# Optimization experiments

Measured on AMD Instinct MI355X. Metric: run time of the kernel, lower is better.

Reference implementation:

```python
import jax, jax.numpy as jnp
import numpy as np

B, C_IN, N, K, UP = 4, 128, 1024, 9, 4
EPS_BN = 1e-5


def _grid():
    # gen_grid(4): num_x=num_y=2, linspace(-0.2,0.2,2) -> (4,2)
    g = jnp.linspace(-0.2, 0.2, 2)
    x, y = jnp.meshgrid(g, g, indexing='ij')
    return jnp.stack([x, y], axis=-1).reshape(-1, 2)


def _knn(x, k, dilation):
    # x: (B,C,N). L2-normalize features, matrix pairwise dist, top-k, dilated select.
    nrm = jnp.sqrt(jnp.sum(x * x, axis=1, keepdims=True))
    xn = x / jnp.maximum(nrm, 1e-12)
    xt = xn.transpose(0, 2, 1)                      # (B,N,C)
    sq = jnp.sum(xt * xt, axis=-1)                  # (B,N)
    dist = sq[:, :, None] - 2.0 * jnp.einsum('bnc,bmc->bnm', xt, xt) + sq[:, None, :]
    _, idx = jax.lax.top_k(-dist, k * dilation)     # k*d nearest (incl. self)
    return idx[:, :, ::dilation]                    # (B,N,k)


def _bn(x, g, b, axes):
    # training-mode batchnorm over given axes, channel axis = 1
    m = jnp.mean(x, axis=axes, keepdims=True)
    v = jnp.mean((x - m) ** 2, axis=axes, keepdims=True)
    sh = [1] * x.ndim
    sh[1] = -1
    return (x - m) * jax.lax.rsqrt(v + EPS_BN) * g.reshape(sh) + b.reshape(sh)


def _edge_conv(x, k, dil, W, g, b):
    # DGCNN edge conv: gather neighbors, [x_i, x_j-x_i], 1x1 conv, BN, relu, max over k
    idx = _knn(x, k, dil)                                        # (B,N,k)
    x_j = jax.vmap(lambda xx, ii: xx[:, ii])(x, idx)             # (B,C,N,k)
    x_i = jnp.broadcast_to(x[..., None], x_j.shape)
    feat = jnp.concatenate([x_i, x_j - x_i], axis=1)             # (B,2C,N,k)
    out = jnp.einsum('oc,bcnk->bonk', W, feat)
    out = jax.nn.relu(_bn(out, g, b, (0, 2, 3)))
    return jnp.max(out, axis=-1)                                 # (B,Cout,N)


def _conv1d(x, W, b):
    return jnp.einsum('oc,bcn->bon', W, x) + b[None, :, None]


def _atten(x, Wf, bf, gf, bef, Wg, bg, gg, beg, Wh, bh, gh, beh, gamma):
    # attention_unit / RA_Layer1 math (C=130)
    f = jax.nn.relu(_bn(_conv1d(x, Wf, bf), gf, bef, (0, 2)))    # (B,C/4,M)
    g_ = jax.nn.relu(_bn(_conv1d(x, Wg, bg), gg, beg, (0, 2)))
    h = jax.nn.relu(_bn(_conv1d(x, Wh, bh), gh, beh, (0, 2)))    # (B,C,M)
    s = jnp.einsum('bcn,bcm->bnm', g_, f)                        # g^T @ f: (B,M,M)
    beta = jax.nn.softmax(s, axis=2)
    o = jnp.einsum('bcn,bnm->bcm', h, beta)                      # h @ beta
    return gamma * o + x


def _forward(inp, Wa, gna, bta, Wb, gnb, btb, Wf, bf, gf, bef, Wg, bg, gg, beg,
             Wh, bh, gh, beh, gamma, W1, b1, W2, b2):
    x1 = _edge_conv(inp, K, 1, Wa, gna, bta)                     # (B,256,N)
    x2 = _edge_conv(inp, K, 2, Wb, gnb, btb)                     # (B,256,N)
    x = jnp.concatenate([x1, x2], axis=1)                        # (B,512,N)
    net = x.transpose(0, 2, 1).reshape(B, N * UP, 128)           # (B,4N,128)
    grid = jnp.repeat(_grid(), N, axis=0)                        # (4N,2)
    grid = jnp.broadcast_to(grid[None], (B, N * UP, 2)).astype(net.dtype)
    net = jnp.concatenate([net, grid], axis=2).transpose(0, 2, 1)  # (B,130,4N)
    net = _atten(net, Wf, bf, gf, bef, Wg, bg, gg, beg, Wh, bh, gh, beh, gamma)
    net = jax.nn.relu(_conv1d(net, W1, b1))                      # 130->256
    net = jax.nn.relu(_conv1d(net, W2, b2))                      # 256->128
    return net                                                   # (B,128,4N)


def setup_inputs() -> dict:
    key = jax.random.key(0)
    ks = jax.random.split(key, 24)
    rn = lambda k, sh, s=0.05: jax.random.normal(k, sh, jnp.float32) * s
    d = {
        'inp': jax.random.normal(ks[0], (B, C_IN, N), jnp.float32),
        'Wa': rn(ks[1], (256, 256)), 'gna': 1.0 + rn(ks[2], (256,)), 'bta': rn(ks[3], (256,)),
        'Wb': rn(ks[4], (256, 256)), 'gnb': 1.0 + rn(ks[5], (256,)), 'btb': rn(ks[6], (256,)),
        'Wf': rn(ks[7], (32, 130)), 'bf': rn(ks[8], (32,)), 'gf': 1.0 + rn(ks[9], (32,)), 'bef': rn(ks[9], (32,)),
        'Wg': rn(ks[10], (32, 130)), 'bg': rn(ks[11], (32,)), 'gg': 1.0 + rn(ks[12], (32,)), 'beg': rn(ks[12], (32,)),
        'Wh': rn(ks[13], (130, 130)), 'bh': rn(ks[14], (130,)), 'gh': 1.0 + rn(ks[15], (130,)), 'beh': rn(ks[15], (130,)),
        'gamma': rn(ks[16], (), 1.0),
        'W1': rn(ks[17], (256, 130)), 'b1': rn(ks[18], (256,)),
        'W2': rn(ks[19], (128, 256)), 'b2': rn(ks[20], (128,)),
    }
    return d


def reference(inp, Wa, gna, bta, Wb, gnb, btb, Wf, bf, gf, bef, Wg, bg, gg, beg,
              Wh, bh, gh, beh, gamma, W1, b1, W2, b2):
    return _forward(inp, Wa, gna, bta, Wb, gnb, btb, Wf, bf, gf, bef, Wg, bg, gg, beg,
                    Wh, bh, gh, beh, gamma, W1, b1, W2, b2)
```

## Files before the change

kernel.cpp:

```cpp
#include <hip/hip_runtime.h>

namespace {
constexpr int NB = 4;
constexpr int CI = 128;
constexpr int NP = 1024;
constexpr int MM = 4096;
constexpr float EPSBN = 1e-5f;
constexpr float LOG2E = 1.4426950408889634f;

constexpr size_t OPS_SH = 2162688;
constexpr size_t OFF_OP   = 0;
constexpr size_t OFF_DIST = 0;
constexpr size_t OFF_PM   = 0;
constexpr size_t OFF_QM   = 2097152;
constexpr size_t OFF_HRAW = 0;
constexpr size_t OFF_FGRAW= 2359296;
constexpr size_t OFF_Y1   = 0;
constexpr size_t OFF_FGT  = 6488064;
constexpr size_t OFF_HB   = 7012352;
constexpr size_t OFF_A16  = 6488064;
constexpr size_t OFF_X16  = 8192000;
constexpr size_t OFF_LSE  = 9502720;
constexpr size_t OFF_LSEP = 9519104;
constexpr size_t OFF_STATS= 9650176;
constexpr size_t OFF_ABE  = 9715712;
constexpr size_t OFF_ABFG = 9716736;
constexpr size_t OFF_ABH  = 9716864;
constexpr size_t OFF_FGP  = 9717376;
constexpr size_t OFF_BIAS = 9725568;
constexpr size_t OFF_W16  = 9726208;
constexpr size_t OFF_KNN  = 9779712;
constexpr size_t OFF_XN   = 9853440;
constexpr size_t OFF_SQ   = 10377728;
constexpr size_t W16_FG = 0;
constexpr size_t W16_H  = 10240;
constexpr size_t W16_C1 = 33280;
constexpr size_t W16_C2 = 74240;
constexpr size_t B_FG = 0, B_H = 64, B_C1 = 208, B_C2 = 464;
}

typedef __attribute__((ext_vector_type(8))) short short8;
typedef __attribute__((ext_vector_type(4))) float f32x4;
#define MFMA16(A, B, C) __builtin_amdgcn_mfma_f32_16x16x32_bf16(A, B, C, 0, 0, 0)

__device__ inline unsigned short f2bf(float x) {
  unsigned int u = __float_as_uint(x);
  unsigned int r = u + 0x7fff + ((u >> 16) & 1);
  return (unsigned short)(r >> 16);
}
__device__ inline float bf2f(unsigned short s) {
  return __uint_as_float(((unsigned int)s) << 16);
}

__global__ __launch_bounds__(256) void k_prep(const float* __restrict__ Wf, const float* __restrict__ Wg,
                                              const float* __restrict__ Wh, const float* __restrict__ W1,
                                              const float* __restrict__ W2, const float* __restrict__ bf,
                                              const float* __restrict__ bg, const float* __restrict__ bh,
                                              const float* __restrict__ b1, const float* __restrict__ b2,
                                              unsigned short* __restrict__ W16, float* __restrict__ BIAS) {
  int i = blockIdx.x * 256 + threadIdx.x;
  if (i < 107008) {
    float v = 0.f;
    if (i < 10240) { int o = i / 160, c = i % 160; if (c < 130) v = (o < 32) ? Wf[o * 130 + c] : Wg[(o - 32) * 130 + c]; }
    else if (i < 33280) { int r = i - 10240; int o = r / 160, c = r % 160; if (o < 130 && c < 130) v = Wh[o * 130 + c]; }
    else if (i < 74240) { int r = i - 33280; int o = r / 160, c = r % 160; if (c < 130) v = W1[o * 130 + c]; }
    else { int r = i - 74240; int o = r / 256, c = r % 256; v = W2[o * 256 + c]; }
    W16[i] = f2bf(v);
  } else if (i < 107648) {
    int j = i - 107008; float v = 0.f;
    if (j < 64) v = (j < 32) ? bf[j] : bg[j - 32];
    else if (j < 208) { int c = j - 64; if (c < 130) v = bh[c]; }
    else if (j < 464) v = b1[j - 208];
    else if (j < 592) v = b2[j - 464];
    BIAS[j] = v;
  }
}

__global__ __launch_bounds__(256) void k_norm(const float* __restrict__ x,
                                              float* __restrict__ xn,
                                              float* __restrict__ sq) {
  int t = blockIdx.x * 256 + threadIdx.x;
  int b = t >> 10, n = t & 1023;
  const float* xb = x + (size_t)b * CI * NP + n;
  float ss = 0.f;
  #pragma unroll 4
  for (int c = 0; c < CI; ++c) { float v = xb[(size_t)c * NP]; ss += v * v; }
  float inv = 1.f / fmaxf(sqrtf(ss), 1e-12f);
  float* xo = xn + (size_t)b * CI * NP + n;
  float s2 = 0.f;
  #pragma unroll 4
  for (int c = 0; c < CI; ++c) { float v = xb[(size_t)c * NP] * inv; xo[(size_t)c * NP] = v; s2 += v * v; }
  sq[t] = s2;
}

__global__ __launch_bounds__(256) void k_dist(const float* __restrict__ xn,
                                              const float* __restrict__ sq,
                                              float* __restrict__ dist) {
  __shared__ float As[32][68], Bs[32][68];
  int t = threadIdx.x;
  int m0 = blockIdx.x * 64, n0 = blockIdx.y * 64, b = blockIdx.z;
  int mg = t & 15, ng = t >> 4;
  float acc[16];
  #pragma unroll
  for (int i = 0; i < 16; ++i) acc[i] = 0.f;
  for (int cc = 0; cc < 128; cc += 32) {
    __syncthreads();
    for (int idx = t; idx < 2048; idx += 256) {
      int c = idx >> 6, j = idx & 63;
      As[c][j] = xn[((size_t)b * CI + cc + c) * NP + n0 + j];
      Bs[c][j] = xn[((size_t)b * CI + cc + c) * NP + m0 + j];
    }
    __syncthreads();
    #pragma unroll
    for (int c = 0; c < 32; ++c) {
      float4 avv = *(const float4*)&As[c][ng * 4];
      float4 bvv = *(const float4*)&Bs[c][mg * 4];
      float a[4] = {avv.x, avv.y, avv.z, avv.w};
      float bb[4] = {bvv.x, bvv.y, bvv.z, bvv.w};
      #pragma unroll
      for (int i = 0; i < 4; ++i)
        #pragma unroll
        for (int j = 0; j < 4; ++j) acc[i * 4 + j] += a[i] * bb[j];
    }
  }
  #pragma unroll
  for (int i = 0; i < 4; ++i) {
    int n = n0 + ng * 4 + i;
    float sn = sq[b * NP + n];
    float4 r;
    r.x = sn + sq[b * NP + m0 + mg * 4 + 0] - 2.f * acc[i * 4 + 0];
    r.y = sn + sq[b * NP + m0 + mg * 4 + 1] - 2.f * acc[i * 4 + 1];
    r.z = sn + sq[b * NP + m0 + mg * 4 + 2] - 2.f * acc[i * 4 + 2];
    r.w = sn + sq[b * NP + m0 + mg * 4 + 3] - 2.f * acc[i * 4 + 3];
    *(float4*)&dist[((size_t)b * NP + n) * NP + m0 + mg * 4] = r;
  }
}

__global__ __launch_bounds__(64) void k_knn(const float* __restrict__ dist,
                                            int* __restrict__ knn) {
  int row = blockIdx.x;
  int l = threadIdx.x;
  const float* dr = dist + (size_t)row * NP;
  float d[16];
  #pragma unroll
  for (int i = 0; i < 16; ++i) d[i] = dr[l + 64 * i];
  for (int s = 0; s < 18; ++s) {
    float best = __builtin_inff(); int bslot = -1;
    #pragma unroll
    for (int i = 0; i < 16; ++i) if (d[i] < best) { best = d[i]; bslot = i; }
    int bidx = (bslot >= 0) ? (l + 64 * bslot) : 0x7fffffff;
    float bd = best; int bi = bidx;
    #pragma unroll
    for (int off = 32; off > 0; off >>= 1) {
      float od = __shfl_xor(bd, off);
      int   oi = __shfl_xor(bi, off);
      if (od < bd || (od == bd && oi < bi)) { bd = od; bi = oi; }
    }
    if (l == 0) knn[row * 18 + s] = bi;
    if ((bi & 63) == l) d[bi >> 6] = __builtin_inff();
  }
}

__global__ __launch_bounds__(256) void k_pq(const float* __restrict__ x,
                                            const float* __restrict__ Wa,
                                            const float* __restrict__ Wb,
                                            float* __restrict__ Pm,
                                            float* __restrict__ Qm) {
  __shared__ float Xs[32][68], Wp[32][68], Wq[32][68];
  int t = threadIdx.x;
  int nt = blockIdx.x, ot = blockIdx.y, bz = blockIdx.z;
  int b = bz >> 1, e = bz & 1;
  const float* W = e ? Wb : Wa;
  int eb = e * 4 + b;
  int mg = t & 15, og = t >> 4;
  float accp[16], accq[16];
  #pragma unroll
  for (int i = 0; i < 16; ++i) { accp[i] = 0.f; accq[i] = 0.f; }
  for (int cc = 0; cc < 128; cc += 32) {
    __syncthreads();
    for (int idx = t; idx < 2048; idx += 256) {
      int c = idx >> 6, n = idx & 63;
      Xs[c][n] = x[((size_t)b * CI + cc + c) * NP + nt * 64 + n];
    }
    for (int idx = t; idx < 2048; idx += 256) {
      int o = idx >> 5, c = idx & 31;
      float w1 = W[(ot * 64 + o) * 256 + cc + c];
      float w2 = W[(ot * 64 + o) * 256 + 128 + cc + c];
      Wp[c][o] = w1 - w2; Wq[c][o] = w2;
    }
    __syncthreads();
    #pragma unroll
    for (int c = 0; c < 32; ++c) {
      float4 xv = *(const float4*)&Xs[c][mg * 4];
      float4 wp = *(const float4*)&Wp[c][og * 4];
      float4 wq = *(const float4*)&Wq[c][og * 4];
      float xa[4] = {xv.x, xv.y, xv.z, xv.w};
      float pa[4] = {wp.x, wp.y, wp.z, wp.w};
      float qa[4] = {wq.x, wq.y, wq.z, wq.w};
      #pragma unroll
      for (int i = 0; i < 4; ++i)
        #pragma unroll
        for (int j = 0; j < 4; ++j) { accp[i * 4 + j] += pa[i] * xa[j]; accq[i * 4 + j] += qa[i] * xa[j]; }
    }
  }
  #pragma unroll
  for (int j = 0; j < 4; ++j) {
    int n = nt * 64 + mg * 4 + j;
    int o0 = ot * 64 + og * 4;
    float4 rp = {accp[j], accp[4 + j], accp[8 + j], accp[12 + j]};
    float4 rq = {accq[j], accq[4 + j], accq[8 + j], accq[12 + j]};
    *(float4*)&Pm[((size_t)eb * 1024 + n) * 256 + o0] = rp;
    *(float4*)&Qm[((size_t)eb * 1024 + n) * 256 + o0] = rq;
  }
}

__global__ __launch_bounds__(256) void k_edge_stats(const float* __restrict__ Pm,
                                                    const float* __restrict__ Qm,
                                                    const int* __restrict__ knn,
                                                    float* __restrict__ stats) {
  int o = threadIdx.x;
  int chunk = blockIdx.x, b = blockIdx.y, e = blockIdx.z;
  int eb = e * 4 + b;
  float s = 0.f, s2 = 0.f;
  for (int nn = 0; nn < 64; ++nn) {
    int n = chunk * 64 + nn;
    float p = Pm[((size_t)eb * 1024 + n) * 256 + o];
    const int* kn = knn + (b * 1024 + n) * 18;
    #pragma unroll
    for (int kk = 0; kk < 9; ++kk) {
      int j = kn[e ? 2 * kk : kk];
      float v = p + Qm[((size_t)eb * 1024 + j) * 256 + o];
      s += v; s2 += v * v;
    }
  }
  size_t idx = ((((size_t)e * 4 + b) * 16 + chunk) * 256 + o) * 2;
  stats[idx] = s; stats[idx + 1] = s2;
}

__global__ __launch_bounds__(256) void k_edge_fin(const float* __restrict__ stats,
                                                  const float* __restrict__ gna, const float* __restrict__ bta,
                                                  const float* __restrict__ gnb, const float* __restrict__ btb,
                                                  float* __restrict__ ab) {
  int i = blockIdx.x * 256 + threadIdx.x;
  if (i >= 512) return;
  int e = i >> 8, o = i & 255;
  float s = 0.f, s2 = 0.f;
  for (int b = 0; b < 4; ++b)
    for (int ch = 0; ch < 16; ++ch) {
      size_t idx = ((((size_t)e * 4 + b) * 16 + ch) * 256 + o) * 2;
      s += stats[idx]; s2 += stats[idx + 1];
    }
  float cnt = 4.0f * 1024.0f * 9.0f;
  float mean = s / cnt;
  float var = s2 / cnt - mean * mean;
  float g = e ? gnb[o] : gna[o];
  float bt = e ? btb[o] : bta[o];
  float alpha = g * rsqrtf(var + EPSBN);
  ab[i * 2] = alpha; ab[i * 2 + 1] = bt - mean * alpha;
}

__global__ __launch_bounds__(256) void k_edge_apply(const float* __restrict__ Pm,
                                                    const float* __restrict__ Qm,
                                                    const int* __restrict__ knn,
                                                    const float* __restrict__ ab,
                                                    unsigned short* __restrict__ X16) {
  __shared__ int knl[18];
  int t = threadIdx.x;
  int n = blockIdx.x, b = blockIdx.y;
  if (t < 18) knl[t] = knn[(b * 1024 + n) * 18 + t];
  __syncthreads();
  int e = t >> 7, oo = t & 127;
  int eb = e * 4 + b;
  const float* Pr = Pm + ((size_t)eb * 1024 + n) * 256;
  const float* Qb = Qm + (size_t)eb * 1024 * 256;
  float p0 = Pr[oo], p1 = Pr[oo + 128];
  float a0 = ab[(e * 256 + oo) * 2], be0 = ab[(e * 256 + oo) * 2 + 1];
  float a1 = ab[(e * 256 + oo + 128) * 2], be1 = ab[(e * 256 + oo + 128) * 2 + 1];
  float mx0 = -__builtin_inff(), mx1 = -__builtin_inff();
  #pragma unroll
  for (int kk = 0; kk < 9; ++kk) {
    int j = knl[e ? 2 * kk : kk];
    const float* Qr = Qb + (size_t)j * 256;
    mx0 = fmaxf(mx0, fmaf(a0, p0 + Qr[oo], be0));
    mx1 = fmaxf(mx1, fmaf(a1, p1 + Qr[oo + 128], be1));
  }
  int u0 = e << 1, u1 = (e << 1) | 1;
  X16[((size_t)b * MM + 4 * n + u0) * 160 + oo] = f2bf(fmaxf(mx0, 0.f));
  X16[((size_t)b * MM + 4 * n + u1) * 160 + oo] = f2bf(fmaxf(mx1, 0.f));
  if (t < 128) {
    int u = t >> 5, c = 128 + (t & 31);
    int gr = n >> 8;
    float v = (c == 128) ? ((gr < 2) ? -0.2f : 0.2f) : (c == 129) ? ((gr & 1) ? 0.2f : -0.2f) : 0.f;
    X16[((size_t)b * MM + 4 * n + u) * 160 + c] = f2bf(v);
  }
}

template <int KSTEPS, int CTPER, int OUTMODE, bool RELU>
__global__ __launch_bounds__(256) void k_convm(const unsigned short* __restrict__ src,
                                               const unsigned short* __restrict__ W16,
                                               const float* __restrict__ bias,
                                               float* __restrict__ dstF,
                                               unsigned short* __restrict__ dstB,
                                               int outld, int rows) {
  constexpr int LD = KSTEPS * 32;
  int t = threadIdx.x; int w = t >> 6; int l = t & 63;
  int lm = l & 15, g = l >> 4;
  int b = blockIdx.z; int ct0 = blockIdx.y * CTPER;
  int srow = blockIdx.x * 64 + w * 16 + lm;
  const unsigned short* sp = src + ((size_t)b * MM + srow) * LD + 8 * g;
  const unsigned short* wp = W16 + ((size_t)ct0 * 16 + lm) * LD + 8 * g;
  f32x4 acc[CTPER];
  #pragma unroll
  for (int i = 0; i < CTPER; ++i) acc[i] = {0.f, 0.f, 0.f, 0.f};
  #pragma unroll
  for (int cc = 0; cc < KSTEPS; ++cc) {
    short8 bfr = *(const short8*)(sp + cc * 32);
    #pragma unroll
    for (int ct = 0; ct < CTPER; ++ct) {
      short8 af = *(const short8*)(wp + (size_t)ct * 16 * LD + cc * 32);
      acc[ct] = MFMA16(af, bfr, acc[ct]);
    }
  }
  #pragma unroll
  for (int ct = 0; ct < CTPER; ++ct) {
    int o0 = (ct0 + ct) * 16 + 4 * g;
    float4 bv = *(const float4*)&bias[o0];
    float v[4] = {acc[ct][0] + bv.x, acc[ct][1] + bv.y, acc[ct][2] + bv.z, acc[ct][3] + bv.w};
    if (RELU) { v[0] = fmaxf(v[0], 0.f); v[1] = fmaxf(v[1], 0.f); v[2] = fmaxf(v[2], 0.f); v[3] = fmaxf(v[3], 0.f); }
    if (OUTMODE == 0) {
      float4 r = {v[0], v[1], v[2], v[3]};
      *(float4*)&dstF[((size_t)b * MM + srow) * outld + o0] = r;
    } else if (OUTMODE == 1) {
      uint2 pk;
      pk.x = (unsigned)f2bf(v[0]) | ((unsigned)f2bf(v[1]) << 16);
      pk.y = (unsigned)f2bf(v[2]) | ((unsigned)f2bf(v[3]) << 16);
      *(uint2*)&dstB[((size_t)b * MM + srow) * outld + o0] = pk;
    } else {
      #pragma unroll
      for (int r = 0; r < 4; ++r)
        dstF[((size_t)b * rows + o0 + r) * MM + srow] = v[r];
    }
  }
}

__global__ __launch_bounds__(256) void k_fgstats(const float* __restrict__ FGraw,
                                                 float* __restrict__ FGP) {
  __shared__ float red[4][64][2];
  int t = threadIdx.x; int c = t & 63, rq = t >> 6;
  int blk = blockIdx.x;
  float s = 0.f, s2 = 0.f;
  for (int k = 0; k < 64; ++k) {
    int r = blk * 256 + rq + 4 * k;
    float v = FGraw[(size_t)r * 64 + c];
    s += v; s2 += v * v;
  }
  red[rq][c][0] = s; red[rq][c][1] = s2;
  __syncthreads();
  if (t < 64) {
    float a = 0.f, a2 = 0.f;
    #pragma unroll
    for (int q = 0; q < 4; ++q) { a += red[q][t][0]; a2 += red[q][t][1]; }
    FGP[((size_t)blk * 64 + t) * 2] = a; FGP[((size_t)blk * 64 + t) * 2 + 1] = a2;
  }
}

__global__ __launch_bounds__(64) void k_fgfin(const float* __restrict__ FGP,
                                              const float* __restrict__ gf, const float* __restrict__ bef,
                                              const float* __restrict__ gg, const float* __restrict__ beg,
                                              float* __restrict__ ab) {
  int c = threadIdx.x;
  float s = 0.f, s2 = 0.f;
  for (int blk = 0; blk < 64; ++blk) { s += FGP[((size_t)blk * 64 + c) * 2]; s2 += FGP[((size_t)blk * 64 + c) * 2 + 1]; }
  float cnt = 16384.f;
  float mean = s / cnt, var = s2 / cnt - mean * mean;
  float gv = (c < 32) ? gf[c] : gg[c - 32];
  float bv = (c < 32) ? bef[c] : beg[c - 32];
  float alpha = gv * rsqrtf(var + EPSBN);
  ab[c * 2] = alpha; ab[c * 2 + 1] = bv - mean * alpha;
}

__global__ __launch_bounds__(256) void k_bnstats(const float* __restrict__ src,
                                                 const float* __restrict__ g,
                                                 const float* __restrict__ be,
                                                 float* __restrict__ ab, int ldC) {
  int o = blockIdx.x;
  int t = threadIdx.x;
  float s = 0.f, s2 = 0.f;
  for (int b = 0; b < NB; ++b) {
    const float* r = src + ((size_t)b * ldC + o) * MM;
    for (int m = t; m < MM; m += 256) { float v = r[m]; s += v; s2 += v * v; }
  }
  __shared__ float rs[256], rs2[256];
  rs[t] = s; rs2[t] = s2;
  __syncthreads();
  for (int off = 128; off > 0; off >>= 1) {
    if (t < off) { rs[t] += rs[t + off]; rs2[t] += rs2[t + off]; }
    __syncthreads();
  }
  if (t == 0) {
    float cnt = 16384.0f;
    float mean = rs[0] / cnt, var = rs2[0] / cnt - mean * mean;
    float alpha = g[o] * rsqrtf(var + EPSBN);
    ab[o * 2] = alpha; ab[o * 2 + 1] = be[o] - mean * alpha;
  }
}

__global__ __launch_bounds__(256) void k_cvtFG(const float* __restrict__ FGraw,
                                               const float* __restrict__ ab,
                                               unsigned short* __restrict__ FGT) {
  int i = blockIdx.x * 256 + threadIdx.x;
  int row = i >> 3, c0 = (i & 7) * 8;
  float vv[8];
  float4 u0 = *(const float4*)&FGraw[(size_t)row * 64 + c0];
  float4 u1 = *(const float4*)&FGraw[(size_t)row * 64 + c0 + 4];
  vv[0] = u0.x; vv[1] = u0.y; vv[2] = u0.z; vv[3] = u0.w;
  vv[4] = u1.x; vv[5] = u1.y; vv[6] = u1.z; vv[7] = u1.w;
  uint4 pk;
  unsigned pw[4];
  #pragma unroll
  for (int h = 0; h < 4; ++h) {
    int c = c0 + 2 * h;
    float a0 = ab[c * 2], b0 = ab[c * 2 + 1];
    float a1 = ab[(c + 1) * 2], b1 = ab[(c + 1) * 2 + 1];
    float x0 = fmaxf(fmaf(a0, vv[2 * h], b0), 0.f);
    float x1 = fmaxf(fmaf(a1, vv[2 * h + 1], b1), 0.f);
    pw[h] = (unsigned)f2bf(x0) | ((unsigned)f2bf(x1) << 16);
  }
  pk.x = pw[0]; pk.y = pw[1]; pk.z = pw[2]; pk.w = pw[3];
  *(uint4*)&FGT[(size_t)row * 64 + c0] = pk;
}

__global__ __launch_bounds__(256) void k_cvtH(const float* __restrict__ src,
                                              const float* __restrict__ ab,
                                              unsigned short* __restrict__ dst) {
  int i = blockIdx.x * 256 + threadIdx.x;
  int m4 = i & 1023; int c = (i >> 10) % 144; int b = i / (144 * 1024);
  ushort4 ov = {0, 0, 0, 0};
  if (c < 130) {
    float4 v = *(const float4*)&src[((size_t)b * 144 + c) * MM + m4 * 4];
    float a = ab[c * 2], be = ab[c * 2 + 1];
    ov.x = f2bf(fmaxf(fmaf(a, v.x, be), 0.f));
    ov.y = f2bf(fmaxf(fmaf(a, v.y, be), 0.f));
    ov.z = f2bf(fmaxf(fmaf(a, v.z, be), 0.f));
    ov.w = f2bf(fmaxf(fmaf(a, v.w, be), 0.f));
  }
  *(ushort4*)&dst[((size_t)b * 144 + c) * MM + m4 * 4] = ov;
}

__global__ __launch_bounds__(256) void k_zlse(const unsigned short* __restrict__ FGT,
                                              float* __restrict__ LSEP) {
  int t = threadIdx.x; int w = t >> 6; int l = t & 63;
  int b = blockIdx.z; int ms = blockIdx.y;
  int n0 = blockIdx.x * 64 + w * 16;
  int lm = l & 15, g = l >> 4;
  f32x4 z4 = {0.f, 0.f, 0.f, 0.f};
  short8 af = *(const short8*)&FGT[((size_t)b * MM + n0 + lm) * 64 + 32 + 8 * g];
  float rm[4], zz[4];
  #pragma unroll
  for (int r = 0; r < 4; ++r) { rm[r] = -__builtin_inff(); zz[r] = 0.f; }
  for (int it = 0; it < 16; ++it) {
    int m0 = ms * 1024 + it * 64;
    short8 bfr[4];
    #pragma unroll
    for (int mi = 0; mi < 4; ++mi)
      bfr[mi] = *(const short8*)&FGT[((size_t)b * MM + m0 + mi * 16 + lm) * 64 + 8 * g];
    #pragma unroll
    for (int mi = 0; mi < 4; ++mi) {
      f32x4 d = MFMA16(af, bfr[mi], z4);
      #pragma unroll
      for (int r = 0; r < 4; ++r) {
        float v = d[r] * LOG2E;
        float nm = fmaxf(rm[r], v);
        zz[r] = zz[r] * exp2f(rm[r] - nm) + exp2f(v - nm);
        rm[r] = nm;
      }
    }
  }
  #pragma unroll
  for (int off = 1; off < 16; off <<= 1) {
    #pragma unroll
    for (int r = 0; r < 4; ++r) {
      float om = __shfl_xor(rm[r], off);
      float oz = __shfl_xor(zz[r], off);
      float nm = fmaxf(rm[r], om);
      zz[r] = zz[r] * exp2f(rm[r] - nm) + oz * exp2f(om - nm);
      rm[r] = nm;
    }
  }
  if (lm == 0) {
    #pragma unroll
    for (int r = 0; r < 4; ++r) {
      int n = n0 + 4 * g + r;
      size_t idx = ((size_t)ms * 16384 + (size_t)b * MM + n) * 2;
      LSEP[idx] = rm[r]; LSEP[idx + 1] = zz[r];
    }
  }
}

__global__ __launch_bounds__(256) void k_lsered(const float* __restrict__ LSEP,
                                                float* __restrict__ LSE) {
  int bn = blockIdx.x * 256 + threadIdx.x;
  float rm = -__builtin_inff(), zz = 0.f;
  #pragma unroll
  for (int ms = 0; ms < 4; ++ms) {
    float m = LSEP[((size_t)ms * 16384 + bn) * 2];
    float z = LSEP[((size_t)ms * 16384 + bn) * 2 + 1];
    float nm = fmaxf(rm, m);
    zz = zz * exp2f(rm - nm) + z * exp2f(m - nm);
    rm = nm;
  }
  LSE[bn] = rm + log2f(zz);
}

__global__ __launch_bounds__(256) void k_omfma(const unsigned short* __restrict__ FGT,
                                               const unsigned short* __restrict__ HB,
                                               const float* __restrict__ LSE,
                                               unsigned short* __restrict__ Opart) {
  int t = threadIdx.x; int w = t >> 6; int l = t & 63;
  int b = blockIdx.y; int split = blockIdx.z;
  int lm = l & 15, g = l >> 4;
  int mcol0 = blockIdx.x * 128 + w * 32 + lm;
  int mcol1 = mcol0 + 16;
  f32x4 z4 = {0.f, 0.f, 0.f, 0.f};
  short8 Ff0 = *(const short8*)&FGT[((size_t)b * MM + mcol0) * 64 + 8 * g];
  short8 Ff1 = *(const short8*)&FGT[((size_t)b * MM + mcol1) * 64 + 8 * g];
  f32x4 acc0[9], acc1[9];
  #pragma unroll
  for (int ct = 0; ct < 9; ++ct) { acc0[ct] = z4; acc1[ct] = z4; }
  const int nchunks = (split < 2) ? 22 : 21;
  const int startc = split * 21 + ((split < 2) ? split : 2);
  const int start = startc * 32;
  const int end = start + nchunks * 32;
  const unsigned short* gptr = FGT + ((size_t)b * MM + lm) * 64 + 32 + 8 * g;
  const unsigned short* hbase = HB + ((size_t)b * 144 + lm) * MM + 8 * g;
  const float* lbase = LSE + (size_t)b * MM + 4 * g;
  int src01 = lm + 16 * (2 * (g & 1));
  int src23 = src01 + 16;
  bool hi = g >= 2;

  short8 a0 = *(const short8*)(gptr + (size_t)start * 64);
  short8 a1 = *(const short8*)(gptr + (size_t)(start + 16) * 64);
  float4 l0 = *(const float4*)(lbase + start);
  float4 l1 = *(const float4*)(lbase + start + 16);

  for (int n0 = start; n0 < end; n0 += 32) {
    const unsigned short* hp = hbase + n0;
    short8 hf[9];
    #pragma unroll
    for (int ct = 0; ct < 9; ++ct) hf[ct] = *(const short8*)(hp + (size_t)ct * 16 * MM);
    f32x4 s00 = MFMA16(a0, Ff0, z4);
    f32x4 s10 = MFMA16(a1, Ff0, z4);
    f32x4 s01 = MFMA16(a0, Ff1, z4);
    f32x4 s11 = MFMA16(a1, Ff1, z4);
    int nn = (n0 + 32 < end) ? (n0 + 32) : start;
    short8 na0 = *(const short8*)(gptr + (size_t)nn * 64);
    short8 na1 = *(const short8*)(gptr + (size_t)(nn + 16) * 64);
    float4 nl0 = *(const float4*)(lbase + nn);
    float4 nl1 = *(const float4*)(lbase + nn + 16);
    float le0[4] = {l0.x, l0.y, l0.z, l0.w};
    float le1[4] = {l1.x, l1.y, l1.z, l1.w};
    unsigned pk00[2], pk10[2], pk01[2], pk11[2];
    #pragma unroll
    for (int h2 = 0; h2 < 2; ++h2) {
      float e00a = exp2f(fmaf(s00[2 * h2], LOG2E, -le0[2 * h2]));
      float e00b = exp2f(fmaf(s00[2 * h2 + 1], LOG2E, -le0[2 * h2 + 1]));
      float e10a = exp2f(fmaf(s10[2 * h2], LOG2E, -le1[2 * h2]));
      float e10b = exp2f(fmaf(s10[2 * h2 + 1], LOG2E, -le1[2 * h2 + 1]));
      float e01a = exp2f(fmaf(s01[2 * h2], LOG2E, -le0[2 * h2]));
      float e01b = exp2f(fmaf(s01[2 * h2 + 1], LOG2E, -le0[2 * h2 + 1]));
      float e11a = exp2f(fmaf(s11[2 * h2], LOG2E, -le1[2 * h2]));
      float e11b = exp2f(fmaf(s11[2 * h2 + 1], LOG2E, -le1[2 * h2 + 1]));
      pk00[h2] = (unsigned)f2bf(e00a) | ((unsigned)f2bf(e00b) << 16);
      pk10[h2] = (unsigned)f2bf(e10a) | ((unsigned)f2bf(e10b) << 16);
      pk01[h2] = (unsigned)f2bf(e01a) | ((unsigned)f2bf(e01b) << 16);
      pk11[h2] = (unsigned)f2bf(e11a) | ((unsigned)f2bf(e11b) << 16);
    }
    a0 = na0; a1 = na1; l0 = nl0; l1 = nl1;
    unsigned a0w = (unsigned)__shfl((int)pk00[0], src01);
    unsigned b0w = (unsigned)__shfl((int)pk10[0], src01);
    unsigned a1w = (unsigned)__shfl((int)pk00[1], src01);
    unsigned b1w = (unsigned)__shfl((int)pk10[1], src01);
    unsigned a2w = (unsigned)__shfl((int)pk00[0], src23);
    unsigned b2w = (unsigned)__shfl((int)pk10[0], src23);
    unsigned a3w = (unsigned)__shfl((int)pk00[1], src23);
    unsigned b3w = (unsigned)__shfl((int)pk10[1], src23);
    union { unsigned u[4]; short8 s; } bu0;
    bu0.u[0] = hi ? b0w : a0w; bu0.u[1] = hi ? b1w : a1w;
    bu0.u[2] = hi ? b2w : a2w; bu0.u[3] = hi ? b3w : a3w;
    short8 bfrag0 = bu0.s;
    unsigned c0w = (unsigned)__shfl((int)pk01[0], src01);
    unsigned d0w = (unsigned)__shfl((int)pk11[0], src01);
    unsigned c1w = (unsigned)__shfl((int)pk01[1], src01);
    unsigned d1w = (unsigned)__shfl((int)pk11[1], src01);
    unsigned c2w = (unsigned)__shfl((int)pk01[0], src23);
    unsigned d2w = (unsigned)__shfl((int)pk11[0], src23);
    unsigned c3w = (unsigned)__shfl((int)pk01[1], src23);
    unsigned d3w = (unsigned)__shfl((int)pk11[1], src23);
    union { unsigned u[4]; short8 s; } bu1;
    bu1.u[0] = hi ? d0w : c0w; bu1.u[1] = hi ? d1w : c1w;
    bu1.u[2] = hi ? d2w : c2w; bu1.u[3] = hi ? d3w : c3w;
    short8 bfrag1 = bu1.s;
    #pragma unroll
    for (int ct = 0; ct < 9; ++ct) {
      acc0[ct] = MFMA16(hf[ct], bfrag0, acc0[ct]);
      acc1[ct] = MFMA16(hf[ct], bfrag1, acc1[ct]);
    }
  }
  unsigned short* op0 = Opart + (size_t)split * OPS_SH + ((size_t)b * MM + mcol0) * 132;
  unsigned short* op1 = Opart + (size_t)split * OPS_SH + ((size_t)b * MM + mcol1) * 132;
  #pragma unroll
  for (int ct = 0; ct < 9; ++ct) {
    int c0 = ct * 16 + 4 * g;
    if (c0 < 132) {
      uint2 p0, p1;
      p0.x = (unsigned)f2bf(acc0[ct][0]) | ((unsigned)f2bf(acc0[ct][1]) << 16);
      p0.y = (unsigned)f2bf(acc0[ct][2]) | ((unsigned)f2bf(acc0[ct][3]) << 16);
      p1.x = (unsigned)f2bf(acc1[ct][0]) | ((unsigned)f2bf(acc1[ct][1]) << 16);
      p1.y = (unsigned)f2bf(acc1[ct][2]) | ((unsigned)f2bf(acc1[ct][3]) << 16);
      *(uint2*)&op0[c0] = p0;
      *(uint2*)&op1[c0] = p1;
    }
  }
}

__global__ __launch_bounds__(256) void k_ored(const unsigned short* __restrict__ Op,
                                              const unsigned short* __restrict__ X16,
                                              const float* __restrict__ gma,
                                              unsigned short* __restrict__ A16) {
  int i = blockIdx.x * 256 + threadIdx.x;
  int row = i / 20, c8 = i % 20;
  int c0 = c8 * 8;
  unsigned short* ap = A16 + (size_t)row * 160 + c0;
  if (c0 >= 136) {
    uint4 z = {0, 0, 0, 0};
    *(uint4*)ap = z;
    return;
  }
  float gm = gma[0];
  float ov[8] = {0.f, 0.f, 0.f, 0.f, 0.f, 0.f, 0.f, 0.f};
  #pragma unroll
  for (int s = 0; s < 6; ++s) {
    const unsigned short* base = Op + (size_t)s * OPS_SH + (size_t)row * 132 + c0;
    uint2 u = *(const uint2*)base;
    ov[0] += bf2f((unsigned short)(u.x & 0xffff));
    ov[1] += bf2f((unsigned short)(u.x >> 16));
    ov[2] += bf2f((unsigned short)(u.y & 0xffff));
    ov[3] += bf2f((unsigned short)(u.y >> 16));
    if (c0 + 4 < 132) {
      uint2 v = *(const uint2*)(base + 4);
      ov[4] += bf2f((unsigned short)(v.x & 0xffff));
      ov[5] += bf2f((unsigned short)(v.x >> 16));
      ov[6] += bf2f((unsigned short)(v.y & 0xffff));
      ov[7] += bf2f((unsigned short)(v.y >> 16));
    }
  }
  short8 xv = *(const short8*)(X16 + (size_t)row * 160 + c0);
  unsigned pw[4];
  #pragma unroll
  for (int h = 0; h < 4; ++h) {
    int ca = c0 + 2 * h, cb = c0 + 2 * h + 1;
    float xa = bf2f((unsigned short)xv[2 * h]);
    float xb = bf2f((unsigned short)xv[2 * h + 1]);
    float va = (ca < 132) ? (gm * ov[2 * h] + xa) : 0.f;
    float vb = (cb < 132) ? (gm * ov[2 * h + 1] + xb) : 0.f;
    pw[h] = (unsigned)f2bf(va) | ((unsigned)f2bf(vb) << 16);
  }
  uint4 pk = {pw[0], pw[1], pw[2], pw[3]};
  *(uint4*)ap = pk;
}

extern "C" void kernel_launch(void* const* d_in, const int* in_sizes, int n_in,
                              void* d_out, int out_size, void* d_ws, size_t ws_size,
                              hipStream_t stream) {
  const float* inp = (const float*)d_in[0];
  const float* Wa  = (const float*)d_in[1];
  const float* gna = (const float*)d_in[2];
  const float* bta = (const float*)d_in[3];
  const float* Wb  = (const float*)d_in[4];
  const float* gnb = (const float*)d_in[5];
  const float* btb = (const float*)d_in[6];
  const float* Wf  = (const float*)d_in[7];
  const float* bf  = (const float*)d_in[8];
  const float* gf  = (const float*)d_in[9];
  const float* bef = (const float*)d_in[10];
  const float* Wg  = (const float*)d_in[11];
  const float* bg  = (const float*)d_in[12];
  const float* gg  = (const float*)d_in[13];
  const float* beg = (const float*)d_in[14];
  const float* Wh  = (const float*)d_in[15];
  const float* bh  = (const float*)d_in[16];
  const float* gh  = (const float*)d_in[17];
  const float* beh = (const float*)d_in[18];
  const float* gamma = (const float*)d_in[19];
  const float* W1  = (const float*)d_in[20];
  const float* b1  = (const float*)d_in[21];
  const float* W2  = (const float*)d_in[22];
  const float* b2  = (const float*)d_in[23];
  float* out = (float*)d_out;

  float* ws = (float*)d_ws;
  float* DIST = ws + OFF_DIST;
  float* PM   = ws + OFF_PM;
  float* QM   = ws + OFF_QM;
  float* HRAW = ws + OFF_HRAW;
  float* FGRAW= ws + OFF_FGRAW;
  unsigned short* OP16 = (unsigned short*)(ws + OFF_OP);
  unsigned short* FGT = (unsigned short*)(ws + OFF_FGT);
  unsigned short* HBB = (unsigned short*)(ws + OFF_HB);
  unsigned short* A16 = (unsigned short*)(ws + OFF_A16);
  unsigned short* X16 = (unsigned short*)(ws + OFF_X16);
  unsigned short* Y1  = (unsigned short*)(ws + OFF_Y1);
  float* LSEB = ws + OFF_LSE;
  float* LSEP = ws + OFF_LSEP;
  float* STATS= ws + OFF_STATS;
  float* ABE  = ws + OFF_ABE;
  float* ABFG = ws + OFF_ABFG;
  float* ABH  = ws + OFF_ABH;
  float* FGP  = ws + OFF_FGP;
  float* BIAS = ws + OFF_BIAS;
  unsigned short* W16 = (unsigned short*)(ws + OFF_W16);
  int*   KNNI = (int*)(ws + OFF_KNN);
  float* XN   = ws + OFF_XN;
  float* SQ   = ws + OFF_SQ;

  k_prep<<<421, 256, 0, stream>>>(Wf, Wg, Wh, W1, W2, bf, bg, bh, b1, b2, W16, BIAS);
  k_norm<<<16, 256, 0, stream>>>(inp, XN, SQ);
  k_dist<<<dim3(16, 16, 4), 256, 0, stream>>>(XN, SQ, DIST);
  k_knn<<<4096, 64, 0, stream>>>(DIST, KNNI);
  k_pq<<<dim3(16, 4, 8), 256, 0, stream>>>(inp, Wa, Wb, PM, QM);
  k_edge_stats<<<dim3(16, 4, 2), 256, 0, stream>>>(PM, QM, KNNI, STATS);
  k_edge_fin<<<2, 256, 0, stream>>>(STATS, gna, bta, gnb, btb, ABE);
  k_edge_apply<<<dim3(1024, 4), 256, 0, stream>>>(PM, QM, KNNI, ABE, X16);
  k_convm<5, 2, 0, false><<<dim3(64, 2, 4), 256, 0, stream>>>(X16, W16 + W16_FG, BIAS + B_FG, FGRAW, nullptr, 64, 0);
  k_convm<5, 3, 2, false><<<dim3(64, 3, 4), 256, 0, stream>>>(X16, W16 + W16_H, BIAS + B_H, HRAW, nullptr, 0, 144);
  k_fgstats<<<64, 256, 0, stream>>>(FGRAW, FGP);
  k_fgfin<<<1, 64, 0, stream>>>(FGP, gf, bef, gg, beg, ABFG);
  k_bnstats<<<130, 256, 0, stream>>>(HRAW, gh, beh, ABH, 144);
  k_cvtFG<<<512, 256, 0, stream>>>(FGRAW, ABFG, FGT);
  k_cvtH<<<2304, 256, 0, stream>>>(HRAW, ABH, HBB);
  k_zlse<<<dim3(64, 4, 4), 256, 0, stream>>>(FGT, LSEP);
  k_lsered<<<64, 256, 0, stream>>>(LSEP, LSEB);
  k_omfma<<<dim3(32, 4, 6), 256, 0, stream>>>(FGT, HBB, LSEB, OP16);
  k_ored<<<1280, 256, 0, stream>>>(OP16, X16, gamma, A16);
  k_convm<5, 8, 1, true><<<dim3(64, 2, 4), 256, 0, stream>>>(A16, W16 + W16_C1, BIAS + B_C1, nullptr, Y1, 256, 0);
  k_convm<8, 4, 2, true><<<dim3(64, 2, 4), 256, 0, stream>>>(Y1, W16 + W16_C2, BIAS + B_C2, out, nullptr, 0, 128);
}
```

Measured before the change: 366.3 us.

## Move edge-conv P/Q projection to bf16 MFMA and streamline softmax exp math

The fp32 LDS-tiled P/Q projection GEMM is replaced by a bf16 MFMA kernel. It reads a bf16 row-major copy of the input, produced in the normalisation kernel, and pre-combined bf16 Wa/Wb weights from a new prep kernel. The log2(e) scale is folded into the f-channel BN affine, so the LSE and attention kernels drop the per-element multiply. The LSE loop now batches four MFMA tiles per max/exp update, and the manual bf16 packing is replaced by the hardware v_cvt_pk_bf16_f32 instruction. Together these cut FP32 ALU work but lower the precision of the P/Q projection and add an extra launch plus workspace.

```diff
diff --git a/kernel.cpp b/kernel.cpp
--- a/kernel.cpp
+++ b/kernel.cpp
@@ -32,6 +32,8 @@
 constexpr size_t OFF_KNN  = 9779712;
 constexpr size_t OFF_XN   = 9853440;
 constexpr size_t OFF_SQ   = 10377728;
+constexpr size_t OFF_XR   = 10381824;
+constexpr size_t OFF_WPQ  = 10643968;
 constexpr size_t W16_FG = 0;
 constexpr size_t W16_H  = 10240;
 constexpr size_t W16_C1 = 33280;
@@ -50,6 +52,11 @@
 }
 __device__ inline float bf2f(unsigned short s) {
   return __uint_as_float(((unsigned int)s) << 16);
+}
+__device__ inline unsigned cvtpk(float lo, float hi) {
+  unsigned r;
+  asm("v_cvt_pk_bf16_f32 %0, %1, %2" : "=v"(r) : "v"(lo), "v"(hi));
+  return r;
 }
 
 __global__ __launch_bounds__(256) void k_prep(const float* __restrict__ Wf, const float* __restrict__ Wg,
@@ -76,8 +83,23 @@
   }
 }
 
+__global__ __launch_bounds__(256) void k_prep2(const float* __restrict__ Wa, const float* __restrict__ Wb,
+                                               unsigned short* __restrict__ WPQ) {
+  int i = blockIdx.x * 256 + threadIdx.x;
+  int e = i >> 16;
+  int rem = i & 65535;
+  int pq = rem >> 15;
+  int rr = rem & 32767;
+  int o = rr >> 7, c = rr & 127;
+  const float* W = e ? Wb : Wa;
+  float w1 = W[o * 256 + c], w2 = W[o * 256 + 128 + c];
+  float v = pq ? w2 : (w1 - w2);
+  WPQ[i] = f2bf(v);
+}
+
 __global__ __launch_bounds__(256) void k_norm(const float* __restrict__ x,
                                               float* __restrict__ xn,
+                                              unsigned short* __restrict__ XR,
                                               float* __restrict__ sq) {
   int t = blockIdx.x * 256 + threadIdx.x;
   int b = t >> 10, n = t & 1023;
@@ -88,8 +110,21 @@
   float inv = 1.f / fmaxf(sqrtf(ss), 1e-12f);
   float* xo = xn + (size_t)b * CI * NP + n;
   float s2 = 0.f;
-  #pragma unroll 4
-  for (int c = 0; c < CI; ++c) { float v = xb[(size_t)c * NP] * inv; xo[(size_t)c * NP] = v; s2 += v * v; }
+  for (int c0 = 0; c0 < 128; c0 += 8) {
+    unsigned rw[4];
+    #pragma unroll
+    for (int j = 0; j < 4; ++j) {
+      float va = xb[(size_t)(c0 + 2 * j) * NP];
+      float vb = xb[(size_t)(c0 + 2 * j + 1) * NP];
+      float na = va * inv, nb = vb * inv;
+      s2 += na * na + nb * nb;
+      xo[(size_t)(c0 + 2 * j) * NP] = na;
+      xo[(size_t)(c0 + 2 * j + 1) * NP] = nb;
+      rw[j] = (unsigned)f2bf(va) | ((unsigned)f2bf(vb) << 16);
+    }
+    uint4 r4 = {rw[0], rw[1], rw[2], rw[3]};
+    *(uint4*)&XR[(size_t)t * 128 + c0] = r4;
+  }
   sq[t] = s2;
 }
 
@@ -161,56 +196,40 @@
   }
 }
 
-__global__ __launch_bounds__(256) void k_pq(const float* __restrict__ x,
-                                            const float* __restrict__ Wa,
-                                            const float* __restrict__ Wb,
-                                            float* __restrict__ Pm,
-                                            float* __restrict__ Qm) {
-  __shared__ float Xs[32][68], Wp[32][68], Wq[32][68];
-  int t = threadIdx.x;
-  int nt = blockIdx.x, ot = blockIdx.y, bz = blockIdx.z;
-  int b = bz >> 1, e = bz & 1;
-  const float* W = e ? Wb : Wa;
+__global__ __launch_bounds__(256) void k_pqm(const unsigned short* __restrict__ XR,
+                                             const unsigned short* __restrict__ WPQ,
+                                             float* __restrict__ Pm,
+                                             float* __restrict__ Qm) {
+  int t = threadIdx.x; int w = t >> 6; int l = t & 63;
+  int lm = l & 15, g = l >> 4;
+  int nt = blockIdx.x, oq = blockIdx.y, z = blockIdx.z;
+  int e = z >> 2, b = z & 3;
+  int srow = nt * 64 + w * 16 + lm;
+  const unsigned short* sp = XR + ((size_t)b * 1024 + srow) * 128 + 8 * g;
+  const unsigned short* wpp = WPQ + ((size_t)(e * 2 + 0) * 256 + oq * 64 + lm) * 128 + 8 * g;
+  const unsigned short* wqq = WPQ + ((size_t)(e * 2 + 1) * 256 + oq * 64 + lm) * 128 + 8 * g;
+  f32x4 accp[4], accq[4];
+  #pragma unroll
+  for (int i = 0; i < 4; ++i) { accp[i] = {0.f, 0.f, 0.f, 0.f}; accq[i] = {0.f, 0.f, 0.f, 0.f}; }
+  #pragma unroll
+  for (int cc = 0; cc < 4; ++cc) {
+    short8 bfr = *(const short8*)(sp + cc * 32);
+    #pragma unroll
+    for (int ct = 0; ct < 4; ++ct) {
+      short8 ap = *(const short8*)(wpp + (size_t)ct * 16 * 128 + cc * 32);
+      accp[ct] = MFMA16(ap, bfr, accp[ct]);
+      short8 aq = *(const short8*)(wqq + (size_t)ct * 16 * 128 + cc * 32);
+      accq[ct] = MFMA16(aq, bfr, accq[ct]);
+    }
+  }
   int eb = e * 4 + b;
-  int mg = t & 15, og = t >> 4;
-  float accp[16], accq[16];
-  #pragma unroll
-  for (int i = 0; i < 16; ++i) { accp[i] = 0.f; accq[i] = 0.f; }
-  for (int cc = 0; cc < 128; cc += 32) {
-    __syncthreads();
-    for (int idx = t; idx < 2048; idx += 256) {
-      int c = idx >> 6, n = idx & 63;
-      Xs[c][n] = x[((size_t)b * CI + cc + c) * NP + nt * 64 + n];
-    }
-    for (int idx = t; idx < 2048; idx += 256) {
-      int o = idx >> 5, c = idx & 31;
-      float w1 = W[(ot * 64 + o) * 256 + cc + c];
-      float w2 = W[(ot * 64 + o) * 256 + 128 + cc + c];
-      Wp[c][o] = w1 - w2; Wq[c][o] = w2;
-    }
-    __syncthreads();
-    #pragma unroll
-    for (int c = 0; c < 32; ++c) {
-      float4 xv = *(const float4*)&Xs[c][mg * 4];
-      float4 wp = *(const float4*)&Wp[c][og * 4];
-      float4 wq = *(const float4*)&Wq[c][og * 4];
-      float xa[4] = {xv.x, xv.y, xv.z, xv.w};
-      float pa[4] = {wp.x, wp.y, wp.z, wp.w};
-      float qa[4] = {wq.x, wq.y, wq.z, wq.w};
-      #pragma unroll
-      for (int i = 0; i < 4; ++i)
-        #pragma unroll
-        for (int j = 0; j < 4; ++j) { accp[i * 4 + j] += pa[i] * xa[j]; accq[i * 4 + j] += qa[i] * xa[j]; }
-    }
-  }
-  #pragma unroll
-  for (int j = 0; j < 4; ++j) {
-    int n = nt * 64 + mg * 4 + j;
-    int o0 = ot * 64 + og * 4;
-    float4 rp = {accp[j], accp[4 + j], accp[8 + j], accp[12 + j]};
-    float4 rq = {accq[j], accq[4 + j], accq[8 + j], accq[12 + j]};
-    *(float4*)&Pm[((size_t)eb * 1024 + n) * 256 + o0] = rp;
-    *(float4*)&Qm[((size_t)eb * 1024 + n) * 256 + o0] = rq;
+  #pragma unroll
+  for (int ct = 0; ct < 4; ++ct) {
+    int o0 = oq * 64 + ct * 16 + 4 * g;
+    float4 rp = {accp[ct][0], accp[ct][1], accp[ct][2], accp[ct][3]};
+    float4 rq = {accq[ct][0], accq[ct][1], accq[ct][2], accq[ct][3]};
+    *(float4*)&Pm[((size_t)eb * 1024 + srow) * 256 + o0] = rp;
+    *(float4*)&Qm[((size_t)eb * 1024 + srow) * 256 + o0] = rq;
   }
 }
 
@@ -332,8 +351,8 @@
       *(float4*)&dstF[((size_t)b * MM + srow) * outld + o0] = r;
     } else if (OUTMODE == 1) {
       uint2 pk;
-      pk.x = (unsigned)f2bf(v[0]) | ((unsigned)f2bf(v[1]) << 16);
-      pk.y = (unsigned)f2bf(v[2]) | ((unsigned)f2bf(v[3]) << 16);
+      pk.x = cvtpk(v[0], v[1]);
+      pk.y = cvtpk(v[2], v[3]);
       *(uint2*)&dstB[((size_t)b * MM + srow) * outld + o0] = pk;
     } else {
       #pragma unroll
@@ -410,6 +429,7 @@
                                                unsigned short* __restrict__ FGT) {
   int i = blockIdx.x * 256 + threadIdx.x;
   int row = i >> 3, c0 = (i & 7) * 8;
+  float sc = (c0 < 32) ? LOG2E : 1.0f;
   float vv[8];
   float4 u0 = *(const float4*)&FGraw[(size_t)row * 64 + c0];
   float4 u1 = *(const float4*)&FGraw[(size_t)row * 64 + c0 + 4];
@@ -420,11 +440,11 @@
   #pragma unroll
   for (int h = 0; h < 4; ++h) {
     int c = c0 + 2 * h;
-    float a0 = ab[c * 2], b0 = ab[c * 2 + 1];
-    float a1 = ab[(c + 1) * 2], b1 = ab[(c + 1) * 2 + 1];
+    float a0 = ab[c * 2] * sc, b0 = ab[c * 2 + 1] * sc;
+    float a1 = ab[(c + 1) * 2] * sc, b1 = ab[(c + 1) * 2 + 1] * sc;
     float x0 = fmaxf(fmaf(a0, vv[2 * h], b0), 0.f);
     float x1 = fmaxf(fmaf(a1, vv[2 * h + 1], b1), 0.f);
-    pw[h] = (unsigned)f2bf(x0) | ((unsigned)f2bf(x1) << 16);
+    pw[h] = cvtpk(x0, x1);
   }
   pk.x = pw[0]; pk.y = pw[1]; pk.z = pw[2]; pk.w = pw[3];
   *(uint4*)&FGT[(size_t)row * 64 + c0] = pk;
@@ -464,16 +484,17 @@
     #pragma unroll
     for (int mi = 0; mi < 4; ++mi)
       bfr[mi] = *(const short8*)&FGT[((size_t)b * MM + m0 + mi * 16 + lm) * 64 + 8 * g];
-    #pragma unroll
-    for (int mi = 0; mi < 4; ++mi) {
-      f32x4 d = MFMA16(af, bfr[mi], z4);
-      #pragma unroll
-      for (int r = 0; r < 4; ++r) {
-        float v = d[r] * LOG2E;
-        float nm = fmaxf(rm[r], v);
-        zz[r] = zz[r] * exp2f(rm[r] - nm) + exp2f(v - nm);
-        rm[r] = nm;
-      }
+    f32x4 d[4];
+    #pragma unroll
+    for (int mi = 0; mi < 4; ++mi) d[mi] = MFMA16(af, bfr[mi], z4);
+    #pragma unroll
+    for (int r = 0; r < 4; ++r) {
+      float tm = fmaxf(fmaxf(d[0][r], d[1][r]), fmaxf(d[2][r], d[3][r]));
+      float nm = fmaxf(rm[r], tm);
+      zz[r] = zz[r] * exp2f(rm[r] - nm)
+            + exp2f(d[0][r] - nm) + exp2f(d[1][r] - nm)
+            + exp2f(d[2][r] - nm) + exp2f(d[3][r] - nm);
+      rm[r] = nm;
     }
   }
   #pragma unroll
@@ -562,18 +583,18 @@
     unsigned pk00[2], pk10[2], pk01[2], pk11[2];
     #pragma unroll
     for (int h2 = 0; h2 < 2; ++h2) {
-      float e00a = exp2f(fmaf(s00[2 * h2], LOG2E, -le0[2 * h2]));
-      float e00b = exp2f(fmaf(s00[2 * h2 + 1], LOG2E, -le0[2 * h2 + 1]));
-      float e10a = exp2f(fmaf(s10[2 * h2], LOG2E, -le1[2 * h2]));
-      float e10b = exp2f(fmaf(s10[2 * h2 + 1], LOG2E, -le1[2 * h2 + 1]));
-      float e01a = exp2f(fmaf(s01[2 * h2], LOG2E, -le0[2 * h2]));
-      float e01b = exp2f(fmaf(s01[2 * h2 + 1], LOG2E, -le0[2 * h2 + 1]));
-      float e11a = exp2f(fmaf(s11[2 * h2], LOG2E, -le1[2 * h2]));
-      float e11b = exp2f(fmaf(s11[2 * h2 + 1], LOG2E, -le1[2 * h2 + 1]));
-      pk00[h2] = (unsigned)f2bf(e00a) | ((unsigned)f2bf(e00b) << 16);
-      pk10[h2] = (unsigned)f2bf(e10a) | ((unsigned)f2bf(e10b) << 16);
-      pk01[h2] = (unsigned)f2bf(e01a) | ((unsigned)f2bf(e01b) << 16);
-      pk11[h2] = (unsigned)f2bf(e11a) | ((unsigned)f2bf(e11b) << 16);
+      float e00a = exp2f(s00[2 * h2] - le0[2 * h2]);
+      float e00b = exp2f(s00[2 * h2 + 1] - le0[2 * h2 + 1]);
+      float e10a = exp2f(s10[2 * h2] - le1[2 * h2]);
+      float e10b = exp2f(s10[2 * h2 + 1] - le1[2 * h2 + 1]);
+      float e01a = exp2f(s01[2 * h2] - le0[2 * h2]);
+      float e01b = exp2f(s01[2 * h2 + 1] - le0[2 * h2 + 1]);
+      float e11a = exp2f(s11[2 * h2] - le1[2 * h2]);
+      float e11b = exp2f(s11[2 * h2 + 1] - le1[2 * h2 + 1]);
+      pk00[h2] = cvtpk(e00a, e00b);
+      pk10[h2] = cvtpk(e10a, e10b);
+      pk01[h2] = cvtpk(e01a, e01b);
+      pk11[h2] = cvtpk(e11a, e11b);
     }
     a0 = na0; a1 = na1; l0 = nl0; l1 = nl1;
     unsigned a0w = (unsigned)__shfl((int)pk00[0], src01);
@@ -613,10 +634,10 @@
     int c0 = ct * 16 + 4 * g;
     if (c0 < 132) {
       uint2 p0, p1;
-      p0.x = (unsigned)f2bf(acc0[ct][0]) | ((unsigned)f2bf(acc0[ct][1]) << 16);
-      p0.y = (unsigned)f2bf(acc0[ct][2]) | ((unsigned)f2bf(acc0[ct][3]) << 16);
-      p1.x = (unsigned)f2bf(acc1[ct][0]) | ((unsigned)f2bf(acc1[ct][1]) << 16);
-      p1.y = (unsigned)f2bf(acc1[ct][2]) | ((unsigned)f2bf(acc1[ct][3]) << 16);
+      p0.x = cvtpk(acc0[ct][0], acc0[ct][1]);
+      p0.y = cvtpk(acc0[ct][2], acc0[ct][3]);
+      p1.x = cvtpk(acc1[ct][0], acc1[ct][1]);
+      p1.y = cvtpk(acc1[ct][2], acc1[ct][3]);
       *(uint2*)&op0[c0] = p0;
       *(uint2*)&op1[c0] = p1;
     }
@@ -721,13 +742,16 @@
   unsigned short* W16 = (unsigned short*)(ws + OFF_W16);
   int*   KNNI = (int*)(ws + OFF_KNN);
   float* XN   = ws + OFF_XN;
+  unsigned short* XR = (unsigned short*)(ws + OFF_XR);
+  unsigned short* WPQ = (unsigned short*)(ws + OFF_WPQ);
   float* SQ   = ws + OFF_SQ;
 
   k_prep<<<421, 256, 0, stream>>>(Wf, Wg, Wh, W1, W2, bf, bg, bh, b1, b2, W16, BIAS);
-  k_norm<<<16, 256, 0, stream>>>(inp, XN, SQ);
+  k_prep2<<<512, 256, 0, stream>>>(Wa, Wb, WPQ);
+  k_norm<<<16, 256, 0, stream>>>(inp, XN, XR, SQ);
   k_dist<<<dim3(16, 16, 4), 256, 0, stream>>>(XN, SQ, DIST);
   k_knn<<<4096, 64, 0, stream>>>(DIST, KNNI);
-  k_pq<<<dim3(16, 4, 8), 256, 0, stream>>>(inp, Wa, Wb, PM, QM);
+  k_pqm<<<dim3(16, 4, 8), 256, 0, stream>>>(XR, WPQ, PM, QM);
   k_edge_stats<<<dim3(16, 4, 2), 256, 0, stream>>>(PM, QM, KNNI, STATS);
   k_edge_fin<<<2, 256, 0, stream>>>(STATS, gna, bta, gnb, btb, ABE);
   k_edge_apply<<<dim3(1024, 4), 256, 0, stream>>>(PM, QM, KNNI, ABE, X16);
```

Result: faster. 352.3 us (-3.8%).
